# Performance work log

Hardware: AMD Instinct MI355X
Metric: run time of the kernel (lower is better)

The kernel has to match this reference:

```python
import jax, jax.numpy as jnp
import numpy as np

B, S, D = 2, 2048, 1024
E, DFF = 8, 4096


def setup_inputs() -> dict:
    key = jax.random.key(0)
    ks = jax.random.split(key, 6)
    scale = 0.02
    x = jax.random.normal(ks[0], (B, S, D), dtype=jnp.float32)
    Wg = jax.random.normal(ks[1], (E, D), dtype=jnp.float32) * scale
    bg = jnp.zeros((E,), dtype=jnp.float32)
    W1 = jax.random.normal(ks[2], (E, DFF, D), dtype=jnp.float32) * scale
    W2 = jax.random.normal(ks[3], (E, D, DFF), dtype=jnp.float32) * scale
    W3 = jax.random.normal(ks[4], (E, DFF, D), dtype=jnp.float32) * scale
    return {"x": x, "Wg": Wg, "bg": bg, "W1": W1, "W2": W2, "W3": W3, "top_k": 2}


def reference(x, Wg, bg, W1, W2, W3, top_k):
    # Flatten tokens: [B,S,D] -> [T,D]
    b, s, d = x.shape
    xt = x.reshape(-1, d)
    T = xt.shape[0]
    num_experts = Wg.shape[0]

    # Router (eval path: no noise). logits: [T,E]
    logits = xt @ Wg.T + bg
    top_vals, top_idx = jax.lax.top_k(logits, top_k)  # [T,k]
    # Scatter top-k logits into -inf canvas, then softmax -> sparse weights
    sparse = jnp.full((T, num_experts), -jnp.inf, dtype=logits.dtype)
    sparse = sparse.at[jnp.arange(T)[:, None], top_idx].set(top_vals)
    weights = jax.nn.softmax(sparse, axis=-1)  # zeros outside top-k

    # Per-expert SwiGLU, expressed as dense grouped GEMMs then masked combine.
    # h: [T,E,dff]
    h = jax.nn.silu(jnp.einsum('td,efd->tef', xt, W1)) * jnp.einsum('td,efd->tef', xt, W3)
    out_e = jnp.einsum('tef,edf->ted', h, W2)  # [T,E,D]
    # Weighted combine; non-top-k experts have weight exactly 0.
    y = jnp.einsum('ted,te->td', out_e, weights)
    return y.reshape(b, s, d)
```

## Files before the change

kernel.cpp:

```cpp
#include <hip/hip_runtime.h>
#include <stdint.h>

#define T_TOK   4096
#define D_MODEL 1024
#define N_EXP   8
#define DFF_    4096
#define MAXN    4096
#define MAXTILE 72

typedef __attribute__((ext_vector_type(8))) short short8;
typedef __attribute__((ext_vector_type(4))) float f32x4;

__device__ __forceinline__ unsigned short f2bf(float f) {
  unsigned u = __float_as_uint(f);
  u += 0x7fffu + ((u >> 16) & 1u);
  return (unsigned short)(u >> 16);
}

__device__ __forceinline__ void gld16(const void* g, void* l) {
  __builtin_amdgcn_global_load_lds(
      (const __attribute__((address_space(1))) void*)g,
      (__attribute__((address_space(3))) void*)l, 16, 0, 0);
}

__global__ void k_init(float* __restrict__ y, int* __restrict__ cnt) {
  size_t i = (size_t)blockIdx.x * blockDim.x + threadIdx.x;
  size_t stride = (size_t)gridDim.x * blockDim.x;
  float4* y4 = (float4*)y;
  const size_t n4 = (size_t)T_TOK * D_MODEL / 4;
  float4 z; z.x = z.y = z.z = z.w = 0.f;
  for (size_t k = i; k < n4; k += stride) y4[k] = z;
  if (i < N_EXP) cnt[i] = 0;
}

__global__ void k_cvt(const float* __restrict__ src, unsigned short* __restrict__ dst, size_t n4) {
  size_t i = (size_t)blockIdx.x * blockDim.x + threadIdx.x;
  size_t stride = (size_t)gridDim.x * blockDim.x;
  const float4* s4 = (const float4*)src;
  for (size_t k = i; k < n4; k += stride) {
    float4 v = s4[k];
    ushort4 o;
    o.x = f2bf(v.x); o.y = f2bf(v.y); o.z = f2bf(v.z); o.w = f2bf(v.w);
    *(ushort4*)(dst + 4 * k) = o;
  }
}

__global__ void k_cvt_x(const float* __restrict__ src, unsigned short* __restrict__ dst) {
  const size_t n4  = (size_t)T_TOK * D_MODEL / 4;
  const size_t np4 = (size_t)(T_TOK + 1) * D_MODEL / 4;
  size_t i = (size_t)blockIdx.x * blockDim.x + threadIdx.x;
  size_t stride = (size_t)gridDim.x * blockDim.x;
  const float4* s4 = (const float4*)src;
  for (size_t k = i; k < np4; k += stride) {
    ushort4 o;
    if (k < n4) {
      float4 v = s4[k];
      o.x = f2bf(v.x); o.y = f2bf(v.y); o.z = f2bf(v.z); o.w = f2bf(v.w);
    } else {
      o.x = o.y = o.z = o.w = 0;
    }
    *(ushort4*)(dst + 4 * k) = o;
  }
}

__global__ void k_router(const float* __restrict__ x, const float* __restrict__ Wg,
                         const float* __restrict__ bg, int* __restrict__ cnt,
                         int* __restrict__ tokList, float* __restrict__ wgtList) {
  int wid = (int)((blockIdx.x * blockDim.x + threadIdx.x) >> 6);
  int l = threadIdx.x & 63;
  const float* xr = x + (size_t)wid * D_MODEL;
  float acc[N_EXP];
#pragma unroll
  for (int e = 0; e < N_EXP; ++e) acc[e] = 0.f;
  for (int i = 0; i < D_MODEL / 64; ++i) {
    int c = i * 64 + l;
    float xv = xr[c];
#pragma unroll
    for (int e = 0; e < N_EXP; ++e) acc[e] += xv * Wg[e * D_MODEL + c];
  }
#pragma unroll
  for (int e = 0; e < N_EXP; ++e) {
    float v = acc[e];
    for (int off = 32; off; off >>= 1) v += __shfl_xor(v, off);
    acc[e] = v;
  }
  if (l == 0) {
    float vals[N_EXP];
#pragma unroll
    for (int e = 0; e < N_EXP; ++e) vals[e] = acc[e] + bg[e];
    int e0 = 0; float v0 = vals[0];
#pragma unroll
    for (int e = 1; e < N_EXP; ++e) if (vals[e] > v0) { v0 = vals[e]; e0 = e; }
    int e1 = -1; float v1 = -3.4e38f;
#pragma unroll
    for (int e = 0; e < N_EXP; ++e) if (e != e0 && vals[e] > v1) { v1 = vals[e]; e1 = e; }
    float t = expf(v1 - v0);
    float z = 1.f / (1.f + t);
    float w0 = z, w1 = t * z;
    int s0 = atomicAdd(&cnt[e0], 1);
    tokList[e0 * MAXN + s0] = wid; wgtList[e0 * MAXN + s0] = w0;
    int s1 = atomicAdd(&cnt[e1], 1);
    tokList[e1 * MAXN + s1] = wid; wgtList[e1 * MAXN + s1] = w1;
  }
}

__global__ void k_pad(const int* __restrict__ cnt, int* __restrict__ rto,
                      int* __restrict__ tokList, float* __restrict__ wgtList) {
  if (threadIdx.x == 0) {
    int acc = 0;
    for (int e = 0; e < N_EXP; ++e) { rto[e] = acc; acc += (cnt[e] + 127) >> 7; }
    rto[N_EXP] = acc;
  }
  for (int e = 0; e < N_EXP; ++e) {
    int c = cnt[e];
    int p = ((c + 127) >> 7) << 7;
    for (int s = c + (int)threadIdx.x; s < p; s += 256) {
      tokList[e * MAXN + s] = T_TOK;
      wgtList[e * MAXN + s] = 0.f;
    }
  }
}

__global__ __launch_bounds__(256, 2) void k_gemm13(
    const unsigned short* __restrict__ xb, const unsigned short* __restrict__ w1b,
    const unsigned short* __restrict__ w3b, unsigned short* __restrict__ hbuf,
    const int* __restrict__ tokList, const int* __restrict__ rto) {
  __shared__ alignas(16) short lsA[4 * 128 * 8];
  __shared__ alignas(16) short lsB1[4 * 128 * 8];
  __shared__ alignas(16) short lsB3[4 * 128 * 8];
  __shared__ int lsTok[128];

  const int by = blockIdx.y;
  if (by >= rto[N_EXP]) return;
  int e = 0;
#pragma unroll
  for (int q = 1; q < N_EXP; ++q) if (rto[q] <= by) e = q;
  const int slot0 = (by - rto[e]) * 128;

  const int tid = threadIdx.x;
  const int w = tid >> 6, l = tid & 63;
  const int lr = l >> 4, lc = l & 15;
  const int wm = w >> 1, wn = w & 1;
  const int bx = blockIdx.x;

  if (tid < 128) lsTok[tid] = tokList[e * MAXN + slot0 + tid];
  __syncthreads();

  const char* xbB = (const char*)xb;
  const char* srcA0 = xbB + (size_t)lsTok[l] * 2048 + w * 16;
  const char* srcA1 = xbB + (size_t)lsTok[64 + l] * 2048 + w * 16;
  const size_t wbase = ((size_t)e * DFF_ + (size_t)bx * 128) * 2048;
  const char* srcB1_0 = (const char*)w1b + wbase + (size_t)l * 2048 + w * 16;
  const char* srcB1_1 = (const char*)w1b + wbase + (size_t)(64 + l) * 2048 + w * 16;
  const char* srcB3_0 = (const char*)w3b + wbase + (size_t)l * 2048 + w * 16;
  const char* srcB3_1 = (const char*)w3b + wbase + (size_t)(64 + l) * 2048 + w * 16;

  char* lsAb  = (char*)lsA  + w * 2048;
  char* lsB1b = (char*)lsB1 + w * 2048;
  char* lsB3b = (char*)lsB3 + w * 2048;

  f32x4 accA[4][4], accB[4][4];
#pragma unroll
  for (int i = 0; i < 4; ++i)
#pragma unroll
    for (int j = 0; j < 4; ++j) {
      accA[i][j] = (f32x4){0.f, 0.f, 0.f, 0.f};
      accB[i][j] = (f32x4){0.f, 0.f, 0.f, 0.f};
    }

  const short* aBase  = &lsA [lr * 1024 + (wm * 64 + lc) * 8];
  const short* b1Base = &lsB1[lr * 1024 + (wn * 64 + lc) * 8];
  const short* b3Base = &lsB3[lr * 1024 + (wn * 64 + lc) * 8];

  for (int kk = 0; kk < D_MODEL / 32; ++kk) {
    const size_t ko = (size_t)kk * 64;
    gld16(srcA0 + ko, lsAb);
    gld16(srcA1 + ko, lsAb + 1024);
    gld16(srcB1_0 + ko, lsB1b);
    gld16(srcB1_1 + ko, lsB1b + 1024);
    gld16(srcB3_0 + ko, lsB3b);
    gld16(srcB3_1 + ko, lsB3b + 1024);
    __syncthreads();
    short8 a[4], b1[4], b3[4];
#pragma unroll
    for (int i = 0; i < 4; ++i) a[i]  = *(const short8*)(aBase + i * 128);
#pragma unroll
    for (int j = 0; j < 4; ++j) b1[j] = *(const short8*)(b1Base + j * 128);
#pragma unroll
    for (int j = 0; j < 4; ++j) b3[j] = *(const short8*)(b3Base + j * 128);
#pragma unroll
    for (int i = 0; i < 4; ++i)
#pragma unroll
      for (int j = 0; j < 4; ++j) {
        accA[i][j] = __builtin_amdgcn_mfma_f32_16x16x32_bf16(a[i], b1[j], accA[i][j], 0, 0, 0);
        accB[i][j] = __builtin_amdgcn_mfma_f32_16x16x32_bf16(a[i], b3[j], accB[i][j], 0, 0, 0);
      }
    __syncthreads();
  }

  const size_t hcol = (size_t)bx * 128 + wn * 64 + lc;
#pragma unroll
  for (int i = 0; i < 4; ++i)
#pragma unroll
    for (int r = 0; r < 4; ++r) {
      int m = wm * 64 + i * 16 + lr * 4 + r;
      unsigned short* hrow = hbuf + ((size_t)by * 128 + m) * DFF_ + hcol;
#pragma unroll
      for (int j = 0; j < 4; ++j) {
        float c1 = accA[i][j][r], c3 = accB[i][j][r];
        float hv = c1 / (1.f + __expf(-c1)) * c3;
        hrow[j * 16] = f2bf(hv);
      }
    }
}

__global__ __launch_bounds__(256, 3) void k_gemm2(
    const unsigned short* __restrict__ hbuf, const unsigned short* __restrict__ w2b,
    float* __restrict__ y, const int* __restrict__ tokList,
    const float* __restrict__ wgtList, const int* __restrict__ rto) {
  __shared__ alignas(16) short lsA[4 * 128 * 8];
  __shared__ alignas(16) short lsB[4 * 128 * 8];
  __shared__ int lsTok[128];
  __shared__ float lsW[128];

  const int by = blockIdx.y;
  if (by >= rto[N_EXP]) return;
  int e = 0;
#pragma unroll
  for (int q = 1; q < N_EXP; ++q) if (rto[q] <= by) e = q;
  const int slot0 = (by - rto[e]) * 128;

  const int tid = threadIdx.x;
  const int w = tid >> 6, l = tid & 63;
  const int lr = l >> 4, lc = l & 15;
  const int wm = w >> 1, wn = w & 1;
  const int bx = blockIdx.x;

  if (tid < 128) {
    lsTok[tid] = tokList[e * MAXN + slot0 + tid];
    lsW[tid]   = wgtList[e * MAXN + slot0 + tid];
  }
  __syncthreads();

  const char* hB = (const char*)hbuf;
  const char* srcA0 = hB + ((size_t)by * 128 + l) * 8192 + w * 16;
  const char* srcA1 = hB + ((size_t)by * 128 + 64 + l) * 8192 + w * 16;
  const char* w2B = (const char*)w2b + ((size_t)e * D_MODEL + (size_t)bx * 128) * 8192;
  const char* srcB0 = w2B + (size_t)l * 8192 + w * 16;
  const char* srcB1 = w2B + (size_t)(64 + l) * 8192 + w * 16;

  char* lsAb = (char*)lsA + w * 2048;
  char* lsBb = (char*)lsB + w * 2048;

  f32x4 acc[4][4];
#pragma unroll
  for (int i = 0; i < 4; ++i)
#pragma unroll
    for (int j = 0; j < 4; ++j) acc[i][j] = (f32x4){0.f, 0.f, 0.f, 0.f};

  const short* aBase = &lsA[lr * 1024 + (wm * 64 + lc) * 8];
  const short* bBase = &lsB[lr * 1024 + (wn * 64 + lc) * 8];

  for (int kk = 0; kk < DFF_ / 32; ++kk) {
    const size_t ko = (size_t)kk * 64;
    gld16(srcA0 + ko, lsAb);
    gld16(srcA1 + ko, lsAb + 1024);
    gld16(srcB0 + ko, lsBb);
    gld16(srcB1 + ko, lsBb + 1024);
    __syncthreads();
    short8 a[4], b[4];
#pragma unroll
    for (int i = 0; i < 4; ++i) a[i] = *(const short8*)(aBase + i * 128);
#pragma unroll
    for (int j = 0; j < 4; ++j) b[j] = *(const short8*)(bBase + j * 128);
#pragma unroll
    for (int i = 0; i < 4; ++i)
#pragma unroll
      for (int j = 0; j < 4; ++j)
        acc[i][j] = __builtin_amdgcn_mfma_f32_16x16x32_bf16(a[i], b[j], acc[i][j], 0, 0, 0);
    __syncthreads();
  }

#pragma unroll
  for (int i = 0; i < 4; ++i)
#pragma unroll
    for (int r = 0; r < 4; ++r) {
      int m = wm * 64 + i * 16 + lr * 4 + r;
      int t = lsTok[m];
      float wv = lsW[m];
      if (t < T_TOK) {
        float* yr = y + (size_t)t * D_MODEL + (size_t)bx * 128 + wn * 64 + lc;
#pragma unroll
        for (int j = 0; j < 4; ++j)
          atomicAdd(yr + j * 16, wv * acc[i][j][r]);
      }
    }
}

extern "C" void kernel_launch(void* const* d_in, const int* in_sizes, int n_in,
                              void* d_out, int out_size, void* d_ws, size_t ws_size,
                              hipStream_t stream) {
  const float* x  = (const float*)d_in[0];
  const float* Wg = (const float*)d_in[1];
  const float* bg = (const float*)d_in[2];
  const float* W1 = (const float*)d_in[3];
  const float* W2 = (const float*)d_in[4];
  const float* W3 = (const float*)d_in[5];
  float* y = (float*)d_out;

  char* ws = (char*)d_ws;
  size_t o = 0;
  auto alloc = [&](size_t bytes) -> char* {
    char* p = ws + o;
    o = (o + bytes + 255) & ~(size_t)255;
    return p;
  };
  unsigned short* xb   = (unsigned short*)alloc((size_t)(T_TOK + 1) * D_MODEL * 2);
  unsigned short* w1b  = (unsigned short*)alloc((size_t)N_EXP * DFF_ * D_MODEL * 2);
  unsigned short* w3b  = (unsigned short*)alloc((size_t)N_EXP * DFF_ * D_MODEL * 2);
  unsigned short* w2b  = (unsigned short*)alloc((size_t)N_EXP * D_MODEL * DFF_ * 2);
  unsigned short* hbuf = (unsigned short*)alloc((size_t)MAXTILE * 128 * DFF_ * 2);
  int*   tok = (int*)alloc((size_t)N_EXP * MAXN * 4);
  float* wgt = (float*)alloc((size_t)N_EXP * MAXN * 4);
  int*   cnt = (int*)alloc(64);
  int*   rto = (int*)alloc(64);
  (void)ws_size; (void)in_sizes; (void)n_in; (void)out_size;

  const size_t wn4 = (size_t)N_EXP * DFF_ * D_MODEL / 4;

  hipLaunchKernelGGL(k_init,  dim3(2048), dim3(256), 0, stream, y, cnt);
  hipLaunchKernelGGL(k_cvt_x, dim3(2048), dim3(256), 0, stream, x, xb);
  hipLaunchKernelGGL(k_cvt,   dim3(4096), dim3(256), 0, stream, W1, w1b, wn4);
  hipLaunchKernelGGL(k_cvt,   dim3(4096), dim3(256), 0, stream, W3, w3b, wn4);
  hipLaunchKernelGGL(k_cvt,   dim3(4096), dim3(256), 0, stream, W2, w2b, wn4);
  hipLaunchKernelGGL(k_router, dim3(T_TOK / 4), dim3(256), 0, stream, x, Wg, bg, cnt, tok, wgt);
  hipLaunchKernelGGL(k_pad,   dim3(1), dim3(256), 0, stream, cnt, rto, tok, wgt);
  hipLaunchKernelGGL(k_gemm13, dim3(32, MAXTILE), dim3(256), 0, stream, xb, w1b, w3b, hbuf, tok, rto);
  hipLaunchKernelGGL(k_gemm2,  dim3(8, MAXTILE), dim3(256), 0, stream, hbuf, w2b, y, tok, wgt, rto);
}
```

Before: 978.8 us.

## Double-buffer LDS in both GEMMs, shrink gemm13 N-tile, split-K gemm2

Both expert GEMMs now keep two LDS buffers, so the async global-to-LDS load of the next K slice is issued before the current slice's MFMAs and one barrier per iteration is dropped. k_gemm13 narrows its N tile from 128 to 64 columns, which halves its accumulators and doubles its grid, and raises the occupancy hint to 3 blocks. k_gemm2 splits the DFF reduction four ways across blockIdx.z, which gives four times as many blocks to fill the GPU. The trade-offs are four times as many atomicAdds on y in gemm2 and more reloads of the A tile in gemm13. The gemm2 prefetch has a possible race: it writes the other buffer while a preceding global_load_lds may still be outstanding, with only one barrier per iteration guarding it.

```diff
diff --git a/kernel.cpp b/kernel.cpp
--- a/kernel.cpp
+++ b/kernel.cpp
@@ -7,6 +7,7 @@
 #define DFF_    4096
 #define MAXN    4096
 #define MAXTILE 72
+#define KSPLIT  4
 
 typedef __attribute__((ext_vector_type(8))) short short8;
 typedef __attribute__((ext_vector_type(4))) float f32x4;
@@ -121,13 +122,13 @@
   }
 }
 
-__global__ __launch_bounds__(256, 2) void k_gemm13(
+__global__ __launch_bounds__(256, 3) void k_gemm13(
     const unsigned short* __restrict__ xb, const unsigned short* __restrict__ w1b,
     const unsigned short* __restrict__ w3b, unsigned short* __restrict__ hbuf,
     const int* __restrict__ tokList, const int* __restrict__ rto) {
-  __shared__ alignas(16) short lsA[4 * 128 * 8];
-  __shared__ alignas(16) short lsB1[4 * 128 * 8];
-  __shared__ alignas(16) short lsB3[4 * 128 * 8];
+  __shared__ alignas(16) short lsA[2][4 * 128 * 8];
+  __shared__ alignas(16) short lsB1[2][4 * 64 * 8];
+  __shared__ alignas(16) short lsB3[2][4 * 64 * 8];
   __shared__ int lsTok[128];
 
   const int by = blockIdx.y;
@@ -149,56 +150,55 @@
   const char* xbB = (const char*)xb;
   const char* srcA0 = xbB + (size_t)lsTok[l] * 2048 + w * 16;
   const char* srcA1 = xbB + (size_t)lsTok[64 + l] * 2048 + w * 16;
-  const size_t wbase = ((size_t)e * DFF_ + (size_t)bx * 128) * 2048;
-  const char* srcB1_0 = (const char*)w1b + wbase + (size_t)l * 2048 + w * 16;
-  const char* srcB1_1 = (const char*)w1b + wbase + (size_t)(64 + l) * 2048 + w * 16;
-  const char* srcB3_0 = (const char*)w3b + wbase + (size_t)l * 2048 + w * 16;
-  const char* srcB3_1 = (const char*)w3b + wbase + (size_t)(64 + l) * 2048 + w * 16;
-
-  char* lsAb  = (char*)lsA  + w * 2048;
-  char* lsB1b = (char*)lsB1 + w * 2048;
-  char* lsB3b = (char*)lsB3 + w * 2048;
-
-  f32x4 accA[4][4], accB[4][4];
+  const size_t wbase = ((size_t)e * DFF_ + (size_t)bx * 64) * 2048;
+  const char* srcB1 = (const char*)w1b + wbase + (size_t)l * 2048 + w * 16;
+  const char* srcB3 = (const char*)w3b + wbase + (size_t)l * 2048 + w * 16;
+
+  f32x4 accA[4][2], accB[4][2];
 #pragma unroll
   for (int i = 0; i < 4; ++i)
 #pragma unroll
-    for (int j = 0; j < 4; ++j) {
+    for (int j = 0; j < 2; ++j) {
       accA[i][j] = (f32x4){0.f, 0.f, 0.f, 0.f};
       accB[i][j] = (f32x4){0.f, 0.f, 0.f, 0.f};
     }
 
-  const short* aBase  = &lsA [lr * 1024 + (wm * 64 + lc) * 8];
-  const short* b1Base = &lsB1[lr * 1024 + (wn * 64 + lc) * 8];
-  const short* b3Base = &lsB3[lr * 1024 + (wn * 64 + lc) * 8];
-
+  auto stage = [&](int kt, int b) {
+    const size_t ko = (size_t)kt * 64;
+    gld16(srcA0 + ko, (char*)lsA[b] + w * 2048);
+    gld16(srcA1 + ko, (char*)lsA[b] + w * 2048 + 1024);
+    gld16(srcB1 + ko, (char*)lsB1[b] + w * 1024);
+    gld16(srcB3 + ko, (char*)lsB3[b] + w * 1024);
+  };
+
+  stage(0, 0);
+  __syncthreads();
+
+  int cur = 0;
   for (int kk = 0; kk < D_MODEL / 32; ++kk) {
-    const size_t ko = (size_t)kk * 64;
-    gld16(srcA0 + ko, lsAb);
-    gld16(srcA1 + ko, lsAb + 1024);
-    gld16(srcB1_0 + ko, lsB1b);
-    gld16(srcB1_1 + ko, lsB1b + 1024);
-    gld16(srcB3_0 + ko, lsB3b);
-    gld16(srcB3_1 + ko, lsB3b + 1024);
-    __syncthreads();
-    short8 a[4], b1[4], b3[4];
+    if (kk + 1 < D_MODEL / 32) stage(kk + 1, cur ^ 1);
+    const short* aBase  = &lsA [cur][lr * 1024 + (wm * 64 + lc) * 8];
+    const short* b1Base = &lsB1[cur][lr * 512 + (wn * 32 + lc) * 8];
+    const short* b3Base = &lsB3[cur][lr * 512 + (wn * 32 + lc) * 8];
+    short8 a[4], b1[2], b3[2];
 #pragma unroll
     for (int i = 0; i < 4; ++i) a[i]  = *(const short8*)(aBase + i * 128);
 #pragma unroll
-    for (int j = 0; j < 4; ++j) b1[j] = *(const short8*)(b1Base + j * 128);
-#pragma unroll
-    for (int j = 0; j < 4; ++j) b3[j] = *(const short8*)(b3Base + j * 128);
+    for (int j = 0; j < 2; ++j) b1[j] = *(const short8*)(b1Base + j * 128);
+#pragma unroll
+    for (int j = 0; j < 2; ++j) b3[j] = *(const short8*)(b3Base + j * 128);
 #pragma unroll
     for (int i = 0; i < 4; ++i)
 #pragma unroll
-      for (int j = 0; j < 4; ++j) {
+      for (int j = 0; j < 2; ++j) {
         accA[i][j] = __builtin_amdgcn_mfma_f32_16x16x32_bf16(a[i], b1[j], accA[i][j], 0, 0, 0);
         accB[i][j] = __builtin_amdgcn_mfma_f32_16x16x32_bf16(a[i], b3[j], accB[i][j], 0, 0, 0);
       }
     __syncthreads();
-  }
-
-  const size_t hcol = (size_t)bx * 128 + wn * 64 + lc;
+    cur ^= 1;
+  }
+
+  const size_t hcol = (size_t)bx * 64 + wn * 32 + lc;
 #pragma unroll
   for (int i = 0; i < 4; ++i)
 #pragma unroll
@@ -206,7 +206,7 @@
       int m = wm * 64 + i * 16 + lr * 4 + r;
       unsigned short* hrow = hbuf + ((size_t)by * 128 + m) * DFF_ + hcol;
 #pragma unroll
-      for (int j = 0; j < 4; ++j) {
+      for (int j = 0; j < 2; ++j) {
         float c1 = accA[i][j][r], c3 = accB[i][j][r];
         float hv = c1 / (1.f + __expf(-c1)) * c3;
         hrow[j * 16] = f2bf(hv);
@@ -218,8 +218,8 @@
     const unsigned short* __restrict__ hbuf, const unsigned short* __restrict__ w2b,
     float* __restrict__ y, const int* __restrict__ tokList,
     const float* __restrict__ wgtList, const int* __restrict__ rto) {
-  __shared__ alignas(16) short lsA[4 * 128 * 8];
-  __shared__ alignas(16) short lsB[4 * 128 * 8];
+  __shared__ alignas(16) short lsA[2][4 * 128 * 8];
+  __shared__ alignas(16) short lsB[2][4 * 128 * 8];
   __shared__ int lsTok[128];
   __shared__ float lsW[128];
 
@@ -235,6 +235,7 @@
   const int lr = l >> 4, lc = l & 15;
   const int wm = w >> 1, wn = w & 1;
   const int bx = blockIdx.x;
+  const int kz = blockIdx.z;
 
   if (tid < 128) {
     lsTok[tid] = tokList[e * MAXN + slot0 + tid];
@@ -242,15 +243,13 @@
   }
   __syncthreads();
 
+  const size_t kzoff = (size_t)kz * 2048;
   const char* hB = (const char*)hbuf;
-  const char* srcA0 = hB + ((size_t)by * 128 + l) * 8192 + w * 16;
-  const char* srcA1 = hB + ((size_t)by * 128 + 64 + l) * 8192 + w * 16;
+  const char* srcA0 = hB + ((size_t)by * 128 + l) * 8192 + w * 16 + kzoff;
+  const char* srcA1 = hB + ((size_t)by * 128 + 64 + l) * 8192 + w * 16 + kzoff;
   const char* w2B = (const char*)w2b + ((size_t)e * D_MODEL + (size_t)bx * 128) * 8192;
-  const char* srcB0 = w2B + (size_t)l * 8192 + w * 16;
-  const char* srcB1 = w2B + (size_t)(64 + l) * 8192 + w * 16;
-
-  char* lsAb = (char*)lsA + w * 2048;
-  char* lsBb = (char*)lsB + w * 2048;
+  const char* srcB0 = w2B + (size_t)l * 8192 + w * 16 + kzoff;
+  const char* srcB1 = w2B + (size_t)(64 + l) * 8192 + w * 16 + kzoff;
 
   f32x4 acc[4][4];
 #pragma unroll
@@ -258,16 +257,23 @@
 #pragma unroll
     for (int j = 0; j < 4; ++j) acc[i][j] = (f32x4){0.f, 0.f, 0.f, 0.f};
 
-  const short* aBase = &lsA[lr * 1024 + (wm * 64 + lc) * 8];
-  const short* bBase = &lsB[lr * 1024 + (wn * 64 + lc) * 8];
-
-  for (int kk = 0; kk < DFF_ / 32; ++kk) {
-    const size_t ko = (size_t)kk * 64;
-    gld16(srcA0 + ko, lsAb);
-    gld16(srcA1 + ko, lsAb + 1024);
-    gld16(srcB0 + ko, lsBb);
-    gld16(srcB1 + ko, lsBb + 1024);
-    __syncthreads();
+  auto stage = [&](int kt, int b) {
+    const size_t ko = (size_t)kt * 64;
+    gld16(srcA0 + ko, (char*)lsA[b] + w * 2048);
+    gld16(srcA1 + ko, (char*)lsA[b] + w * 2048 + 1024);
+    gld16(srcB0 + ko, (char*)lsB[b] + w * 2048);
+    gld16(srcB1 + ko, (char*)lsB[b] + w * 2048 + 1024);
+  };
+
+  stage(0, 0);
+  __syncthreads();
+
+  int cur = 0;
+  const int NIT = DFF_ / KSPLIT / 32;
+  for (int kk = 0; kk < NIT; ++kk) {
+    if (kk + 1 < NIT) stage(kk + 1, cur ^ 1);
+    const short* aBase = &lsA[cur][lr * 1024 + (wm * 64 + lc) * 8];
+    const short* bBase = &lsB[cur][lr * 1024 + (wn * 64 + lc) * 8];
     short8 a[4], b[4];
 #pragma unroll
     for (int i = 0; i < 4; ++i) a[i] = *(const short8*)(aBase + i * 128);
@@ -279,6 +285,7 @@
       for (int j = 0; j < 4; ++j)
         acc[i][j] = __builtin_amdgcn_mfma_f32_16x16x32_bf16(a[i], b[j], acc[i][j], 0, 0, 0);
     __syncthreads();
+    cur ^= 1;
   }
 
 #pragma unroll
@@ -335,6 +342,6 @@
   hipLaunchKernelGGL(k_cvt,   dim3(4096), dim3(256), 0, stream, W2, w2b, wn4);
   hipLaunchKernelGGL(k_router, dim3(T_TOK / 4), dim3(256), 0, stream, x, Wg, bg, cnt, tok, wgt);
   hipLaunchKernelGGL(k_pad,   dim3(1), dim3(256), 0, stream, cnt, rto, tok, wgt);
-  hipLaunchKernelGGL(k_gemm13, dim3(32, MAXTILE), dim3(256), 0, stream, xb, w1b, w3b, hbuf, tok, rto);
-  hipLaunchKernelGGL(k_gemm2,  dim3(8, MAXTILE), dim3(256), 0, stream, hbuf, w2b, y, tok, wgt, rto);
-}
+  hipLaunchKernelGGL(k_gemm13, dim3(DFF_ / 64, MAXTILE), dim3(256), 0, stream, xb, w1b, w3b, hbuf, tok, rto);
+  hipLaunchKernelGGL(k_gemm2,  dim3(D_MODEL / 128, MAXTILE, KSPLIT), dim3(256), 0, stream, hbuf, w2b, y, tok, wgt, rto);
+}
```

Result: slower. 1.027 ms (+4.9%).
